# Kernel optimization log

Measured on AMD Instinct MI355X. Metric: run time of the kernel, lower is better.

## Reference

```python
import jax, jax.numpy as jnp
import numpy as np

NUM_WIRES = 20
BATCH = 32
DIM = 2 ** NUM_WIRES


def setup_inputs() -> dict:
    key = jax.random.key(0)
    k1, k2, k3 = jax.random.split(key, 3)
    state = jax.random.normal(k1, (BATCH, DIM), dtype=jnp.float32)
    state = state / jnp.linalg.norm(state, axis=1, keepdims=True)  # valid quantum states
    params = jax.random.normal(k2, (2 * NUM_WIRES,), dtype=jnp.float32)
    W = jax.random.normal(k3, (1, NUM_WIRES), dtype=jnp.float32) * 0.1
    b = jnp.zeros((1,), dtype=jnp.float32)
    return {"state": state, "params": params, "W": W, "b": b}


def _apply_1q(psi, U, wire):
    # psi: [B, 2^n] complex; apply 2x2 unitary U on `wire` (wire 0 = most significant axis,
    # matching PennyLane's big-endian wire ordering).
    B = psi.shape[0]
    left = 2 ** wire
    psi4 = psi.reshape(B, left, 2, -1)
    psi4 = jnp.einsum('ts,bisj->bitj', U, psi4)
    return psi4.reshape(B, DIM)


def _apply_cnot(psi, ctrl):
    # CNOT on adjacent wires (ctrl, ctrl+1): swap target amplitudes where control=1.
    B = psi.shape[0]
    left = 2 ** ctrl
    psi5 = psi.reshape(B, left, 2, 2, -1)
    top = psi5[:, :, 0]
    bot = psi5[:, :, 1, ::-1]
    return jnp.stack([top, bot], axis=2).reshape(B, DIM)


def _circuit(state, params):
    psi = state.astype(jnp.complex64)
    for i in range(NUM_WIRES):
        # RX(theta_i)
        c = jnp.cos(params[i] / 2).astype(jnp.complex64)
        s = jnp.sin(params[i] / 2)
        RX = jnp.stack([jnp.stack([c, -1j * s]), jnp.stack([-1j * s, c])])
        psi = _apply_1q(psi, RX, i)
        # RY(theta_{i+n})
        c2 = jnp.cos(params[i + NUM_WIRES] / 2).astype(jnp.complex64)
        s2 = jnp.sin(params[i + NUM_WIRES] / 2).astype(jnp.complex64)
        RY = jnp.stack([jnp.stack([c2, -s2]), jnp.stack([s2, c2])])
        psi = _apply_1q(psi, RY, i)
    for i in range(NUM_WIRES - 1):
        psi = _apply_cnot(psi, i)
    # <Z_i> = sum over basis states of |amp|^2 * (+1 if bit_i==0 else -1)
    probs = psi.real ** 2 + psi.imag ** 2  # [B, 2^n] float32
    B = probs.shape[0]
    feats = []
    for i in range(NUM_WIRES):
        p = probs.reshape(B, 2 ** i, 2, -1)
        feats.append(p[:, :, 0].sum(axis=(1, 2)) - p[:, :, 1].sum(axis=(1, 2)))
    return jnp.stack(feats, axis=1)  # [B, n]


def reference(state, params, W, b):
    feats = _circuit(state, params)          # [B, num_wires]
    out = feats @ W.T + b                    # Linear head
    return out.squeeze(-1)                   # [B]
```

## Files before the change

### kernel.cpp

```cpp
#include <hip/hip_runtime.h>
#include <hip/hip_fp16.h>

#define NW 20

typedef _Float16 h2 __attribute__((ext_vector_type(2)));
typedef float    f4 __attribute__((ext_vector_type(4)));

struct PkW7 { h2 a, d, dn, e, en, f, fn, pad; };

__device__ __forceinline__ h2 pkrtz(float lo, float hi) {
    typedef __fp16 f16x2 __attribute__((ext_vector_type(2)));
    f16x2 v = __builtin_amdgcn_cvt_pkrtz(lo, hi);
    return *reinterpret_cast<h2*>(&v);
}
__device__ __forceinline__ unsigned h2u(h2 v) { return *reinterpret_cast<unsigned*>(&v); }
__device__ __forceinline__ h2 u2h(unsigned v) { return *reinterpret_cast<h2*>(&v); }

template<int JB>
__device__ __forceinline__ void stage16s(h2 (&xr)[16], h2 (&xi)[16], const PkW7 u) {
    #pragma unroll
    for (int base = 0; base < 16; ++base)
        if (!(base & (1 << JB))) {
            const int p = base | (1 << JB);
            h2 x0r = xr[base], x0i = xi[base], x1r = xr[p], x1i = xi[p];
            xr[base] = u.a * x0r + u.dn * x0i + u.en * x1r + u.f  * x1i;
            xi[base] = u.a * x0i + u.d  * x0r + u.en * x1i + u.fn * x1r;
            xr[p]    = u.e * x0r + u.f  * x0i + u.a  * x1r + u.d  * x1i;
            xi[p]    = u.e * x0i + u.fn * x0r + u.a  * x1i + u.dn * x1r;
        }
}

template<int JB>
__device__ __forceinline__ void shufstage(h2 (&xr)[16], h2 (&xi)[16], const PkW7 u, int t) {
    const bool hi_ = (t >> JB) & 1;
    const h2 ds_  = hi_ ? u.d  : u.dn;
    const h2 nds_ = hi_ ? u.dn : u.d;
    const h2 es_  = hi_ ? u.e  : u.en;
    #pragma unroll
    for (int r = 0; r < 16; ++r) {
        h2 or_ = xr[r], oi_ = xi[r];
        int pri = __shfl_xor(*reinterpret_cast<int*>(&or_), 1 << JB, 64);
        int pii = __shfl_xor(*reinterpret_cast<int*>(&oi_), 1 << JB, 64);
        h2 pr_ = *reinterpret_cast<h2*>(&pri);
        h2 pi_ = *reinterpret_cast<h2*>(&pii);
        xr[r] = u.a * or_ + ds_  * oi_ + es_ * pr_ + u.f  * pi_;
        xi[r] = u.a * oi_ + nds_ * or_ + es_ * pi_ + u.fn * pr_;
    }
}

__global__ void setupk(const float* __restrict__ params, float* __restrict__ cbuf) {
    int w = threadIdx.x;
    if (w < NW) {
        double s1, c1, s2, c2;
        sincos(0.5 * (double)params[w],      &s1, &c1);
        sincos(0.5 * (double)params[w + NW], &s2, &c2);
        float a = (float)(c1 * c2), d = (float)(s1 * s2);
        float e = (float)(s2 * c1), f = (float)(c2 * s1);
        if (w == 19) {
            cbuf[0] = a * 1024.f; cbuf[1] = d * 1024.f;
            cbuf[2] = e * 1024.f; cbuf[3] = f * 1024.f;
        }
        PkW7 pw;
        pw.a.x  = (_Float16) a; pw.a.y  = (_Float16) a;
        pw.d.x  = (_Float16) d; pw.d.y  = (_Float16) d;
        pw.dn.x = (_Float16)-d; pw.dn.y = (_Float16)-d;
        pw.e.x  = (_Float16) e; pw.e.y  = (_Float16) e;
        pw.en.x = (_Float16)-e; pw.en.y = (_Float16)-e;
        pw.f.x  = (_Float16) f; pw.f.y  = (_Float16) f;
        pw.fn.x = (_Float16)-f; pw.fn.y = (_Float16)-f;
        pw.pad.x = (_Float16)0.f; pw.pad.y = (_Float16)0.f;
        ((PkW7*)(cbuf + 4))[w] = pw;
    }
}

__global__ __launch_bounds__(256, 8) void pass1(const float* __restrict__ state,
                                                const float* __restrict__ cbuf,
                                                uint2* __restrict__ amp) {
    __shared__ h2 L[4224];
    const int t     = threadIdx.x;
    const int pr    = blockIdx.x >> 8;
    const int chunk = blockIdx.x & 255;
    const PkW7* PW = (const PkW7*)(cbuf + 4);
    const float a19 = cbuf[0], d19 = cbuf[1], e19 = cbuf[2], f19 = cbuf[3];

    const f4* s0 = (const f4*)(state + ((size_t)pr << 20) + ((size_t)chunk << 12));
    const f4* s1 = (const f4*)((const float*)s0 + ((size_t)16 << 20));

    h2 xr[16], xi[16];
    #pragma unroll
    for (int k = 0; k < 4; ++k) {
        f4 v0 = __builtin_nontemporal_load(s0 + k * 256 + t);
        f4 v1 = __builtin_nontemporal_load(s1 + k * 256 + t);
        float r0a = fmaf(a19, v0.x, -e19 * v0.y), i0a = fmaf( d19, v0.x, -f19 * v0.y);
        float r1a = fmaf(e19, v0.x,  a19 * v0.y), i1a = fmaf(-f19, v0.x, -d19 * v0.y);
        float r0b = fmaf(a19, v1.x, -e19 * v1.y), i0b = fmaf( d19, v1.x, -f19 * v1.y);
        float r1b = fmaf(e19, v1.x,  a19 * v1.y), i1b = fmaf(-f19, v1.x, -d19 * v1.y);
        xr[4*k+0] = pkrtz(r0a, r0b); xi[4*k+0] = pkrtz(i0a, i0b);
        xr[4*k+1] = pkrtz(r1a, r1b); xi[4*k+1] = pkrtz(i1a, i1b);
        r0a = fmaf(a19, v0.z, -e19 * v0.w); i0a = fmaf( d19, v0.z, -f19 * v0.w);
        r1a = fmaf(e19, v0.z,  a19 * v0.w); i1a = fmaf(-f19, v0.z, -d19 * v0.w);
        r0b = fmaf(a19, v1.z, -e19 * v1.w); i0b = fmaf( d19, v1.z, -f19 * v1.w);
        r1b = fmaf(e19, v1.z,  a19 * v1.w); i1b = fmaf(-f19, v1.z, -d19 * v1.w);
        xr[4*k+2] = pkrtz(r0a, r0b); xi[4*k+2] = pkrtz(i0a, i0b);
        xr[4*k+3] = pkrtz(r1a, r1b); xi[4*k+3] = pkrtz(i1a, i1b);
    }
    stage16s<1>(xr, xi, PW[18]);
    stage16s<2>(xr, xi, PW[9]);
    stage16s<3>(xr, xi, PW[8]);

    shufstage<0>(xr, xi, PW[17], t);
    shufstage<1>(xr, xi, PW[16], t);
    shufstage<2>(xr, xi, PW[15], t);
    shufstage<3>(xr, xi, PW[14], t);
    shufstage<4>(xr, xi, PW[13], t);
    shufstage<5>(xr, xi, PW[12], t);

    const int p1 = 4 * t + (t >> 3);
    const int q  = (t & 63) + ((t & 63) >> 5) + 1056 * (t >> 6);
    #pragma unroll
    for (int r = 0; r < 16; ++r) L[p1 + (r & 3) + 1056 * (r >> 2)] = xr[r];
    __syncthreads();
    #pragma unroll
    for (int r = 0; r < 16; ++r) xr[r] = L[q + 66 * (r & 3) + 264 * (r >> 2)];
    __syncthreads();
    #pragma unroll
    for (int r = 0; r < 16; ++r) L[p1 + (r & 3) + 1056 * (r >> 2)] = xi[r];
    __syncthreads();
    #pragma unroll
    for (int r = 0; r < 16; ++r) xi[r] = L[q + 66 * (r & 3) + 264 * (r >> 2)];

    stage16s<2>(xr, xi, PW[11]);
    stage16s<3>(xr, xi, PW[10]);

    uint2* dst = amp + ((size_t)pr << 20) + ((size_t)chunk << 12);
    const int sb = (t & 63) + 1024 * (t >> 6);
    #pragma unroll
    for (int r = 0; r < 16; ++r) {
        uint2 w; w.x = h2u(xr[r]); w.y = h2u(xi[r]);
        dst[sb + 64 * (r & 3) + 256 * (r >> 2)] = w;
    }
}

__global__ __launch_bounds__(256, 8) void pass2(const uint2* __restrict__ amp,
                                                const float* __restrict__ cbuf,
                                                const float* __restrict__ Wv,
                                                float* __restrict__ pws) {
    __shared__ h2     L[4224];
    __shared__ float2 Asig[256];
    __shared__ float  Btab[16];
    __shared__ float  wred[8];
    const int t        = threadIdx.x;
    const int pr       = blockIdx.x >> 8;
    const int chunk    = blockIdx.x & 255;
    const int low_base = chunk * 16;
    const int l = t & 15, hi = t >> 4;
    const PkW7* PW = (const PkW7*)(cbuf + 4);

    {
        float A = 0.f;
        #pragma unroll
        for (int i = 0; i < 8; ++i)
            A += Wv[i] * (1.f - 2.f * (float)(__popc(t >> (7 - i)) & 1));
        Asig[t] = make_float2(A, 1.f - 2.f * (float)(__popc(t) & 1));
    }
    if (t < 16) {
        int low = low_base + t;
        float Bs = 0.f;
        #pragma unroll
        for (int i = 8; i < 20; ++i)
            Bs += Wv[i] * (1.f - 2.f * (float)(__popc(low >> (19 - i)) & 1));
        Btab[t] = Bs;
    }

    const uint2* src = amp + ((size_t)pr << 20) + low_base + l;
    h2 xr[16], xi[16];
    #pragma unroll
    for (int r = 0; r < 16; ++r) {
        uint2 w = src[(size_t)(hi * 16 + r) * 4096];
        xr[r] = u2h(w.x); xi[r] = u2h(w.y);
    }
    stage16s<0>(xr, xi, PW[7]);
    stage16s<1>(xr, xi, PW[6]);
    stage16s<2>(xr, xi, PW[5]);
    stage16s<3>(xr, xi, PW[4]);

    const int p = 264 * hi + l;
    const int q = t + (t >> 5);
    #pragma unroll
    for (int r = 0; r < 16; ++r) L[p + 16 * r + (r >> 1)] = xr[r];
    __syncthreads();
    #pragma unroll
    for (int r = 0; r < 16; ++r) xr[r] = L[q + 264 * r];
    __syncthreads();
    #pragma unroll
    for (int r = 0; r < 16; ++r) L[p + 16 * r + (r >> 1)] = xi[r];
    __syncthreads();
    #pragma unroll
    for (int r = 0; r < 16; ++r) xi[r] = L[q + 264 * r];

    stage16s<0>(xr, xi, PW[3]);
    stage16s<1>(xr, xi, PW[2]);
    stage16s<2>(xr, xi, PW[1]);
    stage16s<3>(xr, xi, PW[0]);

    const float Bl = Btab[l];
    float acc0 = 0.f, acc1 = 0.f;
    #pragma unroll
    for (int r = 0; r < 16; ++r) {
        float vrx = (float)xr[r].x, vry = (float)xr[r].y;
        float vix = (float)xi[r].x, viy = (float)xi[r].y;
        float2 as = Asig[r * 16 + hi];
        float g = fmaf(as.y, Bl, as.x);
        acc0 = fmaf(fmaf(vrx, vrx, vix * vix), g, acc0);
        acc1 = fmaf(fmaf(vry, vry, viy * viy), g, acc1);
    }
    #pragma unroll
    for (int off = 32; off > 0; off >>= 1) {
        acc0 += __shfl_down(acc0, off, 64);
        acc1 += __shfl_down(acc1, off, 64);
    }
    if ((t & 63) == 0) { wred[(t >> 6) * 2] = acc0; wred[(t >> 6) * 2 + 1] = acc1; }
    __syncthreads();
    if (t < 2)
        pws[blockIdx.x * 2 + t] = (wred[t] + wred[2 + t]) + (wred[4 + t] + wred[6 + t]);
}

__global__ void finalk(const float* __restrict__ pws, const float* __restrict__ bias,
                       float* __restrict__ out) {
    const int t = threadIdx.x;
    const int b = t >> 3, j = t & 7;
    const int pr = b & 15, sl = b >> 4;
    float s = 0.f;
    #pragma unroll 4
    for (int k = 0; k < 32; ++k) {
        const int c = j * 32 + k;
        s += pws[(pr * 256 + c) * 2 + sl];
    }
    s += __shfl_down(s, 4, 8);
    s += __shfl_down(s, 2, 8);
    s += __shfl_down(s, 1, 8);
    if (j == 0) out[b] = s * (1.f / 1048576.f) + bias[0];
}

extern "C" void kernel_launch(void* const* d_in, const int* in_sizes, int n_in,
                              void* d_out, int out_size, void* d_ws, size_t ws_size,
                              hipStream_t stream) {
    const float* state  = (const float*)d_in[0];
    const float* params = (const float*)d_in[1];
    const float* Wv     = (const float*)d_in[2];
    const float* bias   = (const float*)d_in[3];
    float* out = (float*)d_out;

    const size_t AMPB = (size_t)16 * (1u << 20) * 8;
    uint2* amp  = (uint2*)d_ws;
    float* pws  = (float*)((char*)d_ws + AMPB);
    float* cbuf = (float*)((char*)d_ws + AMPB + 65536);

    setupk<<<1, 64, 0, stream>>>(params, cbuf);
    pass1 <<<16 * 256, 256, 0, stream>>>(state, cbuf, amp);
    pass2 <<<16 * 256, 256, 0, stream>>>(amp, cbuf, Wv, pws);
    finalk<<<1, 256, 0, stream>>>(pws, bias, out);
}
```

Measured before the change: 109.3 us.

## Double-buffer pass1 input via global_load_lds and process two chunks per block

pass1 now stages its fp32 state input into shared memory with asynchronous global-to-LDS loads. Each block handles two chunks and prefetches the second while computing the first, with half as many blocks launched. Two of the wave-shuffle butterfly stages are replaced by in-register stages after the LDS transpose, which cuts cross-lane shuffle work. The larger shared-memory footprint lowers occupancy (launch bounds 3), and the correctness of the changed stage mapping depends on the transpose layout.

```diff
diff --git a/kernel.cpp b/kernel.cpp
--- a/kernel.cpp
+++ b/kernel.cpp
@@ -15,6 +15,16 @@
 }
 __device__ __forceinline__ unsigned h2u(h2 v) { return *reinterpret_cast<unsigned*>(&v); }
 __device__ __forceinline__ h2 u2h(unsigned v) { return *reinterpret_cast<h2*>(&v); }
+
+__device__ __forceinline__ void glds16(const float* g, float* l) {
+    __builtin_amdgcn_global_load_lds(
+        (const __attribute__((address_space(1))) void*)g,
+        (__attribute__((address_space(3))) void*)l, 16, 0, 0);
+}
+__device__ __forceinline__ void lds_barrier() {
+    asm volatile("s_waitcnt lgkmcnt(0)" ::: "memory");
+    __builtin_amdgcn_s_barrier();
+}
 
 template<int JB>
 __device__ __forceinline__ void stage16s(h2 (&xr)[16], h2 (&xi)[16], const PkW7 u) {
@@ -73,71 +83,111 @@
     }
 }
 
-__global__ __launch_bounds__(256, 8) void pass1(const float* __restrict__ state,
+__global__ __launch_bounds__(256, 3) void pass1(const float* __restrict__ state,
                                                 const float* __restrict__ cbuf,
                                                 uint2* __restrict__ amp) {
-    __shared__ h2 L[4224];
-    const int t     = threadIdx.x;
-    const int pr    = blockIdx.x >> 8;
-    const int chunk = blockIdx.x & 255;
+    __shared__ float SMEM[8192 + 4224];
+    float* stg = SMEM;
+    h2*    L   = reinterpret_cast<h2*>(SMEM + 8192);
+    const int t  = threadIdx.x;
+    const int pr = blockIdx.x >> 7;
+    const int gg = blockIdx.x & 127;
     const PkW7* PW = (const PkW7*)(cbuf + 4);
     const float a19 = cbuf[0], d19 = cbuf[1], e19 = cbuf[2], f19 = cbuf[3];
 
-    const f4* s0 = (const f4*)(state + ((size_t)pr << 20) + ((size_t)chunk << 12));
-    const f4* s1 = (const f4*)((const float*)s0 + ((size_t)16 << 20));
-
-    h2 xr[16], xi[16];
-    #pragma unroll
-    for (int k = 0; k < 4; ++k) {
-        f4 v0 = __builtin_nontemporal_load(s0 + k * 256 + t);
-        f4 v1 = __builtin_nontemporal_load(s1 + k * 256 + t);
-        float r0a = fmaf(a19, v0.x, -e19 * v0.y), i0a = fmaf( d19, v0.x, -f19 * v0.y);
-        float r1a = fmaf(e19, v0.x,  a19 * v0.y), i1a = fmaf(-f19, v0.x, -d19 * v0.y);
-        float r0b = fmaf(a19, v1.x, -e19 * v1.y), i0b = fmaf( d19, v1.x, -f19 * v1.y);
-        float r1b = fmaf(e19, v1.x,  a19 * v1.y), i1b = fmaf(-f19, v1.x, -d19 * v1.y);
-        xr[4*k+0] = pkrtz(r0a, r0b); xi[4*k+0] = pkrtz(i0a, i0b);
-        xr[4*k+1] = pkrtz(r1a, r1b); xi[4*k+1] = pkrtz(i1a, i1b);
-        r0a = fmaf(a19, v0.z, -e19 * v0.w); i0a = fmaf( d19, v0.z, -f19 * v0.w);
-        r1a = fmaf(e19, v0.z,  a19 * v0.w); i1a = fmaf(-f19, v0.z, -d19 * v0.w);
-        r0b = fmaf(a19, v1.z, -e19 * v1.w); i0b = fmaf( d19, v1.z, -f19 * v1.w);
-        r1b = fmaf(e19, v1.z,  a19 * v1.w); i1b = fmaf(-f19, v1.z, -d19 * v1.w);
-        xr[4*k+2] = pkrtz(r0a, r0b); xi[4*k+2] = pkrtz(i0a, i0b);
-        xr[4*k+3] = pkrtz(r1a, r1b); xi[4*k+3] = pkrtz(i1a, i1b);
-    }
-    stage16s<1>(xr, xi, PW[18]);
-    stage16s<2>(xr, xi, PW[9]);
-    stage16s<3>(xr, xi, PW[8]);
-
-    shufstage<0>(xr, xi, PW[17], t);
-    shufstage<1>(xr, xi, PW[16], t);
-    shufstage<2>(xr, xi, PW[15], t);
-    shufstage<3>(xr, xi, PW[14], t);
-    shufstage<4>(xr, xi, PW[13], t);
-    shufstage<5>(xr, xi, PW[12], t);
-
-    const int p1 = 4 * t + (t >> 3);
-    const int q  = (t & 63) + ((t & 63) >> 5) + 1056 * (t >> 6);
-    #pragma unroll
-    for (int r = 0; r < 16; ++r) L[p1 + (r & 3) + 1056 * (r >> 2)] = xr[r];
-    __syncthreads();
-    #pragma unroll
-    for (int r = 0; r < 16; ++r) xr[r] = L[q + 66 * (r & 3) + 264 * (r >> 2)];
-    __syncthreads();
-    #pragma unroll
-    for (int r = 0; r < 16; ++r) L[p1 + (r & 3) + 1056 * (r >> 2)] = xi[r];
-    __syncthreads();
-    #pragma unroll
-    for (int r = 0; r < 16; ++r) xi[r] = L[q + 66 * (r & 3) + 264 * (r >> 2)];
-
-    stage16s<2>(xr, xi, PW[11]);
-    stage16s<3>(xr, xi, PW[10]);
-
-    uint2* dst = amp + ((size_t)pr << 20) + ((size_t)chunk << 12);
-    const int sb = (t & 63) + 1024 * (t >> 6);
-    #pragma unroll
-    for (int r = 0; r < 16; ++r) {
-        uint2 w; w.x = h2u(xr[r]); w.y = h2u(xi[r]);
-        dst[sb + 64 * (r & 3) + 256 * (r >> 2)] = w;
+    const float* base0 = state + ((size_t)pr << 20);
+    const float* base1 = base0 + ((size_t)16 << 20);
+    const int w  = t >> 6, ln = t & 63;
+
+    {
+        const float* c0b0 = base0 + ((size_t)gg << 12);
+        const float* c0b1 = base1 + ((size_t)gg << 12);
+        #pragma unroll
+        for (int m = 0; m < 8; ++m) {
+            const int sg = m * 4 + w;
+            const int off = ((sg & 15) << 8) + (ln << 2);
+            glds16((sg < 16 ? c0b0 : c0b1) + off, &stg[(sg << 8) + (ln << 2)]);
+        }
+    }
+
+    #pragma unroll
+    for (int j = 0; j < 2; ++j) {
+        const int c = gg + 128 * j;
+        asm volatile("s_waitcnt vmcnt(0)" ::: "memory");
+        __builtin_amdgcn_s_barrier();
+
+        f4 va[4], vb[4];
+        #pragma unroll
+        for (int k = 0; k < 4; ++k) {
+            va[k] = *reinterpret_cast<const f4*>(&stg[k * 1024 + 4 * t]);
+            vb[k] = *reinterpret_cast<const f4*>(&stg[4096 + k * 1024 + 4 * t]);
+        }
+        lds_barrier();
+
+        if (j == 0) {
+            const float* c1b0 = base0 + ((size_t)(gg + 128) << 12);
+            const float* c1b1 = base1 + ((size_t)(gg + 128) << 12);
+            #pragma unroll
+            for (int m = 0; m < 8; ++m) {
+                const int sg = m * 4 + w;
+                const int off = ((sg & 15) << 8) + (ln << 2);
+                glds16((sg < 16 ? c1b0 : c1b1) + off, &stg[(sg << 8) + (ln << 2)]);
+            }
+        }
+
+        h2 xr[16], xi[16];
+        #pragma unroll
+        for (int k = 0; k < 4; ++k) {
+            f4 v0 = va[k], v1 = vb[k];
+            float r0a = fmaf(a19, v0.x, -e19 * v0.y), i0a = fmaf( d19, v0.x, -f19 * v0.y);
+            float r1a = fmaf(e19, v0.x,  a19 * v0.y), i1a = fmaf(-f19, v0.x, -d19 * v0.y);
+            float r0b = fmaf(a19, v1.x, -e19 * v1.y), i0b = fmaf( d19, v1.x, -f19 * v1.y);
+            float r1b = fmaf(e19, v1.x,  a19 * v1.y), i1b = fmaf(-f19, v1.x, -d19 * v1.y);
+            xr[4*k+0] = pkrtz(r0a, r0b); xi[4*k+0] = pkrtz(i0a, i0b);
+            xr[4*k+1] = pkrtz(r1a, r1b); xi[4*k+1] = pkrtz(i1a, i1b);
+            r0a = fmaf(a19, v0.z, -e19 * v0.w); i0a = fmaf( d19, v0.z, -f19 * v0.w);
+            r1a = fmaf(e19, v0.z,  a19 * v0.w); i1a = fmaf(-f19, v0.z, -d19 * v0.w);
+            r0b = fmaf(a19, v1.z, -e19 * v1.w); i0b = fmaf( d19, v1.z, -f19 * v1.w);
+            r1b = fmaf(e19, v1.z,  a19 * v1.w); i1b = fmaf(-f19, v1.z, -d19 * v1.w);
+            xr[4*k+2] = pkrtz(r0a, r0b); xi[4*k+2] = pkrtz(i0a, i0b);
+            xr[4*k+3] = pkrtz(r1a, r1b); xi[4*k+3] = pkrtz(i1a, i1b);
+        }
+        stage16s<1>(xr, xi, PW[18]);
+        stage16s<2>(xr, xi, PW[9]);
+        stage16s<3>(xr, xi, PW[8]);
+
+        shufstage<0>(xr, xi, PW[17], t);
+        shufstage<1>(xr, xi, PW[16], t);
+        shufstage<2>(xr, xi, PW[15], t);
+        shufstage<3>(xr, xi, PW[14], t);
+
+        const int p1 = 4 * t + (t >> 3);
+        const int q  = (t & 63) + ((t & 63) >> 5) + 1056 * (t >> 6);
+        #pragma unroll
+        for (int r = 0; r < 16; ++r) L[p1 + (r & 3) + 1056 * (r >> 2)] = xr[r];
+        lds_barrier();
+        #pragma unroll
+        for (int r = 0; r < 16; ++r) xr[r] = L[q + 66 * (r & 3) + 264 * (r >> 2)];
+        lds_barrier();
+        #pragma unroll
+        for (int r = 0; r < 16; ++r) L[p1 + (r & 3) + 1056 * (r >> 2)] = xi[r];
+        lds_barrier();
+        #pragma unroll
+        for (int r = 0; r < 16; ++r) xi[r] = L[q + 66 * (r & 3) + 264 * (r >> 2)];
+
+        stage16s<0>(xr, xi, PW[13]);
+        stage16s<1>(xr, xi, PW[12]);
+        stage16s<2>(xr, xi, PW[11]);
+        stage16s<3>(xr, xi, PW[10]);
+
+        uint2* dst = amp + ((size_t)pr << 20) + ((size_t)c << 12);
+        const int sb = (t & 63) + 1024 * (t >> 6);
+        #pragma unroll
+        for (int r = 0; r < 16; ++r) {
+            uint2 wv; wv.x = h2u(xr[r]); wv.y = h2u(xi[r]);
+            dst[sb + 64 * (r & 3) + 256 * (r >> 2)] = wv;
+        }
+        if (j == 0) lds_barrier();
     }
 }
 
@@ -257,7 +307,7 @@
     float* cbuf = (float*)((char*)d_ws + AMPB + 65536);
 
     setupk<<<1, 64, 0, stream>>>(params, cbuf);
-    pass1 <<<16 * 256, 256, 0, stream>>>(state, cbuf, amp);
+    pass1 <<<16 * 128, 256, 0, stream>>>(state, cbuf, amp);
     pass2 <<<16 * 256, 256, 0, stream>>>(amp, cbuf, Wv, pws);
     finalk<<<1, 256, 0, stream>>>(pws, bias, out);
 }
```

New measurement: 121.9 us. +11.6%, slower.

## Reassign qubit stages between passes to drop shared-memory transpose from pass1

Applied to the files above, without the earlier changes.

Pass1 now handles a different set of wires, using register stages and wave shuffles only, so its LDS transpose and barriers are gone. The global writes change to wide uint4 stores. Pass2 takes over wires 8-11 through shuffles and regroups its reads by a strided quarter index, with a rebuilt sign table for the weighted Z-sum. Launch bounds drop to 4 waves/SIMD. The risks are strided 8-byte gathers in pass2 and lower occupancy.

```diff
diff --git a/kernel.cpp b/kernel.cpp
--- a/kernel.cpp
+++ b/kernel.cpp
@@ -73,144 +73,136 @@
     }
 }
 
-__global__ __launch_bounds__(256, 8) void pass1(const float* __restrict__ state,
+__global__ __launch_bounds__(256, 4) void pass1(const float* __restrict__ state,
                                                 const float* __restrict__ cbuf,
                                                 uint2* __restrict__ amp) {
-    __shared__ h2 L[4224];
-    const int t     = threadIdx.x;
-    const int pr    = blockIdx.x >> 8;
-    const int chunk = blockIdx.x & 255;
+    const int t    = threadIdx.x;
+    const int pr   = blockIdx.x >> 8;
+    const int cgrp = blockIdx.x & 255;
+    const int w = t >> 6, ln = t & 63;
+    const int cc = 4 * cgrp + w;
     const PkW7* PW = (const PkW7*)(cbuf + 4);
     const float a19 = cbuf[0], d19 = cbuf[1], e19 = cbuf[2], f19 = cbuf[3];
 
-    const f4* s0 = (const f4*)(state + ((size_t)pr << 20) + ((size_t)chunk << 12));
-    const f4* s1 = (const f4*)((const float*)s0 + ((size_t)16 << 20));
+    const float* base0 = state + ((size_t)pr << 20) + ((size_t)cc << 8);
+    const float* base1 = base0 + ((size_t)16 << 20);
 
     h2 xr[16], xi[16];
     #pragma unroll
-    for (int k = 0; k < 4; ++k) {
-        f4 v0 = __builtin_nontemporal_load(s0 + k * 256 + t);
-        f4 v1 = __builtin_nontemporal_load(s1 + k * 256 + t);
+    for (int q = 0; q < 4; ++q) {
+        f4 v0 = ((const f4*)(base0 + ((size_t)q << 18)))[ln];
+        f4 v1 = ((const f4*)(base1 + ((size_t)q << 18)))[ln];
         float r0a = fmaf(a19, v0.x, -e19 * v0.y), i0a = fmaf( d19, v0.x, -f19 * v0.y);
         float r1a = fmaf(e19, v0.x,  a19 * v0.y), i1a = fmaf(-f19, v0.x, -d19 * v0.y);
         float r0b = fmaf(a19, v1.x, -e19 * v1.y), i0b = fmaf( d19, v1.x, -f19 * v1.y);
         float r1b = fmaf(e19, v1.x,  a19 * v1.y), i1b = fmaf(-f19, v1.x, -d19 * v1.y);
-        xr[4*k+0] = pkrtz(r0a, r0b); xi[4*k+0] = pkrtz(i0a, i0b);
-        xr[4*k+1] = pkrtz(r1a, r1b); xi[4*k+1] = pkrtz(i1a, i1b);
+        xr[4*q+0] = pkrtz(r0a, r0b); xi[4*q+0] = pkrtz(i0a, i0b);
+        xr[4*q+1] = pkrtz(r1a, r1b); xi[4*q+1] = pkrtz(i1a, i1b);
         r0a = fmaf(a19, v0.z, -e19 * v0.w); i0a = fmaf( d19, v0.z, -f19 * v0.w);
         r1a = fmaf(e19, v0.z,  a19 * v0.w); i1a = fmaf(-f19, v0.z, -d19 * v0.w);
         r0b = fmaf(a19, v1.z, -e19 * v1.w); i0b = fmaf( d19, v1.z, -f19 * v1.w);
         r1b = fmaf(e19, v1.z,  a19 * v1.w); i1b = fmaf(-f19, v1.z, -d19 * v1.w);
-        xr[4*k+2] = pkrtz(r0a, r0b); xi[4*k+2] = pkrtz(i0a, i0b);
-        xr[4*k+3] = pkrtz(r1a, r1b); xi[4*k+3] = pkrtz(i1a, i1b);
+        xr[4*q+2] = pkrtz(r0a, r0b); xi[4*q+2] = pkrtz(i0a, i0b);
+        xr[4*q+3] = pkrtz(r1a, r1b); xi[4*q+3] = pkrtz(i1a, i1b);
     }
     stage16s<1>(xr, xi, PW[18]);
-    stage16s<2>(xr, xi, PW[9]);
-    stage16s<3>(xr, xi, PW[8]);
-
     shufstage<0>(xr, xi, PW[17], t);
     shufstage<1>(xr, xi, PW[16], t);
     shufstage<2>(xr, xi, PW[15], t);
     shufstage<3>(xr, xi, PW[14], t);
     shufstage<4>(xr, xi, PW[13], t);
     shufstage<5>(xr, xi, PW[12], t);
-
-    const int p1 = 4 * t + (t >> 3);
-    const int q  = (t & 63) + ((t & 63) >> 5) + 1056 * (t >> 6);
-    #pragma unroll
-    for (int r = 0; r < 16; ++r) L[p1 + (r & 3) + 1056 * (r >> 2)] = xr[r];
-    __syncthreads();
-    #pragma unroll
-    for (int r = 0; r < 16; ++r) xr[r] = L[q + 66 * (r & 3) + 264 * (r >> 2)];
-    __syncthreads();
-    #pragma unroll
-    for (int r = 0; r < 16; ++r) L[p1 + (r & 3) + 1056 * (r >> 2)] = xi[r];
-    __syncthreads();
-    #pragma unroll
-    for (int r = 0; r < 16; ++r) xi[r] = L[q + 66 * (r & 3) + 264 * (r >> 2)];
-
-    stage16s<2>(xr, xi, PW[11]);
-    stage16s<3>(xr, xi, PW[10]);
-
-    uint2* dst = amp + ((size_t)pr << 20) + ((size_t)chunk << 12);
-    const int sb = (t & 63) + 1024 * (t >> 6);
-    #pragma unroll
-    for (int r = 0; r < 16; ++r) {
-        uint2 w; w.x = h2u(xr[r]); w.y = h2u(xi[r]);
-        dst[sb + 64 * (r & 3) + 256 * (r >> 2)] = w;
-    }
-}
-
-__global__ __launch_bounds__(256, 8) void pass2(const uint2* __restrict__ amp,
+    stage16s<2>(xr, xi, PW[1]);
+    stage16s<3>(xr, xi, PW[0]);
+
+    uint2* dstb = amp + ((size_t)pr << 20) + ((size_t)cc << 8);
+    #pragma unroll
+    for (int q = 0; q < 4; ++q) {
+        uint4* d4 = (uint4*)(dstb + ((size_t)q << 18));
+        uint4 wa, wb;
+        wa.x = h2u(xr[4*q+0]); wa.y = h2u(xi[4*q+0]);
+        wa.z = h2u(xr[4*q+1]); wa.w = h2u(xi[4*q+1]);
+        wb.x = h2u(xr[4*q+2]); wb.y = h2u(xi[4*q+2]);
+        wb.z = h2u(xr[4*q+3]); wb.w = h2u(xi[4*q+3]);
+        d4[2*ln]     = wa;
+        d4[2*ln + 1] = wb;
+    }
+}
+
+__global__ __launch_bounds__(256, 4) void pass2(const uint2* __restrict__ amp,
                                                 const float* __restrict__ cbuf,
                                                 const float* __restrict__ Wv,
                                                 float* __restrict__ pws) {
-    __shared__ h2     L[4224];
-    __shared__ float2 Asig[256];
-    __shared__ float  Btab[16];
-    __shared__ float  wred[8];
-    const int t        = threadIdx.x;
-    const int pr       = blockIdx.x >> 8;
-    const int chunk    = blockIdx.x & 255;
-    const int low_base = chunk * 16;
-    const int l = t & 15, hi = t >> 4;
+    __shared__ h2    L[4224];
+    __shared__ float Atab[1024];
+    __shared__ float wred[8];
+    const int t    = threadIdx.x;
+    const int pr   = blockIdx.x >> 8;
+    const int rest = blockIdx.x & 255;
+    const int cbl  = rest >> 2, q = rest & 3;
     const PkW7* PW = (const PkW7*)(cbuf + 4);
-
-    {
-        float A = 0.f;
+    const float sq  = (__popc(q) & 1) ? -1.f : 1.f;
+    const float sq1 = (q >> 1) ? -1.f : 1.f;
+
+    #pragma unroll
+    for (int mm = t; mm < 1024; mm += 256) {
+        float A = Wv[1];
         #pragma unroll
-        for (int i = 0; i < 8; ++i)
-            A += Wv[i] * (1.f - 2.f * (float)(__popc(t >> (7 - i)) & 1));
-        Asig[t] = make_float2(A, 1.f - 2.f * (float)(__popc(t) & 1));
-    }
-    if (t < 16) {
-        int low = low_base + t;
-        float Bs = 0.f;
-        #pragma unroll
-        for (int i = 8; i < 20; ++i)
-            Bs += Wv[i] * (1.f - 2.f * (float)(__popc(low >> (19 - i)) & 1));
-        Btab[t] = Bs;
-    }
-
-    const uint2* src = amp + ((size_t)pr << 20) + low_base + l;
+        for (int i = 2; i <= 10; ++i)
+            A += Wv[i] * (1.f - 2.f * (float)(__popc(mm >> (11 - i)) & 1));
+        Atab[mm] = fmaf(sq, A, Wv[0] * sq1);
+    }
+    const int l8 = 4 * cbl + (t & 3);
+    float Bl = Wv[11];
+    #pragma unroll
+    for (int i = 12; i <= 19; ++i)
+        Bl += Wv[i] * (1.f - 2.f * (float)(__popc(l8 >> (19 - i)) & 1));
+    Bl *= sq;
+
+    const int mb03 = (t >> 2) & 15, w = t >> 6;
+    const uint2* src = amp + ((size_t)pr << 20) + ((size_t)q << 18) + 4 * cbl + (t & 3);
     h2 xr[16], xi[16];
     #pragma unroll
     for (int r = 0; r < 16; ++r) {
-        uint2 w = src[(size_t)(hi * 16 + r) * 4096];
-        xr[r] = u2h(w.x); xi[r] = u2h(w.y);
-    }
+        const int m = mb03 + 16 * (r & 3) + 64 * (r >> 2) + 256 * w;
+        uint2 v = src[(size_t)m << 8];
+        xr[r] = u2h(v.x); xi[r] = u2h(v.y);
+    }
+    shufstage<2>(xr, xi, PW[11], t);
+    shufstage<3>(xr, xi, PW[10], t);
+    shufstage<4>(xr, xi, PW[9],  t);
+    shufstage<5>(xr, xi, PW[8],  t);
     stage16s<0>(xr, xi, PW[7]);
     stage16s<1>(xr, xi, PW[6]);
     stage16s<2>(xr, xi, PW[5]);
     stage16s<3>(xr, xi, PW[4]);
 
-    const int p = 264 * hi + l;
-    const int q = t + (t >> 5);
-    #pragma unroll
-    for (int r = 0; r < 16; ++r) L[p + 16 * r + (r >> 1)] = xr[r];
-    __syncthreads();
-    #pragma unroll
-    for (int r = 0; r < 16; ++r) xr[r] = L[q + 264 * r];
-    __syncthreads();
-    #pragma unroll
-    for (int r = 0; r < 16; ++r) L[p + 16 * r + (r >> 1)] = xi[r];
-    __syncthreads();
-    #pragma unroll
-    for (int r = 0; r < 16; ++r) xi[r] = L[q + 264 * r];
-
-    stage16s<0>(xr, xi, PW[3]);
-    stage16s<1>(xr, xi, PW[2]);
-    stage16s<2>(xr, xi, PW[1]);
-    stage16s<3>(xr, xi, PW[0]);
-
-    const float Bl = Btab[l];
+    const int pb = (t & 63) + ((t & 63) >> 5);
+    #pragma unroll
+    for (int r = 0; r < 16; ++r) L[pb + 66 * r + 1056 * w] = xr[r];
+    __syncthreads();
+    #pragma unroll
+    for (int r = 0; r < 16; ++r) xr[r] = L[pb + 66 * w + 264 * r];
+    __syncthreads();
+    #pragma unroll
+    for (int r = 0; r < 16; ++r) L[pb + 66 * r + 1056 * w] = xi[r];
+    __syncthreads();
+    #pragma unroll
+    for (int r = 0; r < 16; ++r) xi[r] = L[pb + 66 * w + 264 * r];
+
+    stage16s<2>(xr, xi, PW[3]);
+    stage16s<3>(xr, xi, PW[2]);
+
+    const int mbase = mb03 + 16 * w;
+    const float s_tw = (__popc(mbase) & 1) ? -1.f : 1.f;
     float acc0 = 0.f, acc1 = 0.f;
     #pragma unroll
     for (int r = 0; r < 16; ++r) {
+        const int m = mbase + 64 * (r & 3) + 256 * (r >> 2);
+        const float sg = (__popc(r) & 1) ? -s_tw : s_tw;
+        const float g  = fmaf(sg, Bl, Atab[m]);
         float vrx = (float)xr[r].x, vry = (float)xr[r].y;
         float vix = (float)xi[r].x, viy = (float)xi[r].y;
-        float2 as = Asig[r * 16 + hi];
-        float g = fmaf(as.y, Bl, as.x);
         acc0 = fmaf(fmaf(vrx, vrx, vix * vix), g, acc0);
         acc1 = fmaf(fmaf(vry, vry, viy * viy), g, acc1);
     }
@@ -219,7 +211,7 @@
         acc0 += __shfl_down(acc0, off, 64);
         acc1 += __shfl_down(acc1, off, 64);
     }
-    if ((t & 63) == 0) { wred[(t >> 6) * 2] = acc0; wred[(t >> 6) * 2 + 1] = acc1; }
+    if ((t & 63) == 0) { wred[w * 2] = acc0; wred[w * 2 + 1] = acc1; }
     __syncthreads();
     if (t < 2)
         pws[blockIdx.x * 2 + t] = (wred[t] + wred[2 + t]) + (wred[4 + t] + wred[6 + t]);
```

After: 123.2 us. +12.7%, slower.
